# Kernel optimization log

Measured on AMD Instinct MI355X. Metric: run time of the kernel, lower is better.

Reference implementation:

```python
import jax, jax.numpy as jnp
import numpy as np

# ---- static hash-grid config (mirrors init_kwargs) ----
RANGE = 1.0
DIM = 3
N_LEVELS = 16
F_PER_LEVEL = 2
LOG2_HASHMAP = 15
HASHMAP_SIZE = 1 << LOG2_HASHMAP
BASE_RES = 16
FINEST_RES = 512
RANK = 4
PRIMES = np.array([1, 2654435761, 805459861], dtype=np.uint32)


def _resolutions():
    # N_l = floor(base * b^l), b = exp((ln(Nmax)-ln(Nmin))/(L-1))  (Instant-NGP eq. 2-3)
    b = np.exp((np.log(FINEST_RES) - np.log(BASE_RES)) / (N_LEVELS - 1))
    return np.floor(BASE_RES * b ** np.arange(N_LEVELS)).astype(np.float32)


def setup_inputs() -> dict:
    key = jax.random.key(0)
    k1, k2, k3 = jax.random.split(key, 3)
    x = jax.random.uniform(k1, (524288, DIM), dtype=jnp.float32)  # in [-range, range]
    # LoRA factors; small init like hash-grid tables (~1e-2 scale)
    table_A = jax.random.normal(k2, (N_LEVELS, HASHMAP_SIZE, RANK), dtype=jnp.float32) * 1e-2
    table_B = jax.random.normal(k3, (N_LEVELS, RANK, F_PER_LEVEL), dtype=jnp.float32) * 1e-1
    return {"x": x, "table_A": table_A, "table_B": table_B}


def reference(x, table_A, table_B):
    # wrapper: normalize to [0,1]
    xn = (x + RANGE) / (2.0 * RANGE)                         # [N,3]
    res = jnp.asarray(_resolutions())                        # [L]

    # materialize tiny per-level tables from LoRA factors: [L, S, F]
    tables = jnp.einsum('lsr,lrf->lsf', table_A, table_B)

    xl = xn[None, :, :] * res[:, None, None]                 # [L,N,3]
    xf = jnp.floor(xl)
    w = xl - xf                                              # [L,N,3] trilinear weights
    xi = xf.astype(jnp.uint32)                               # [L,N,3]

    # 2^3 corner offsets
    corners = jnp.array([[(c >> d) & 1 for d in range(DIM)] for c in range(2 ** DIM)],
                        dtype=jnp.uint32)                    # [8,3]

    pos = xi[:, :, None, :] + corners[None, None, :, :]      # [L,N,8,3]
    primes = jnp.asarray(PRIMES)
    h = (pos[..., 0] * primes[0]) ^ (pos[..., 1] * primes[1]) ^ (pos[..., 2] * primes[2])
    idx = (h & jnp.uint32(HASHMAP_SIZE - 1)).astype(jnp.int32)  # [L,N,8]

    # per-level gather: [L,N,8,F]
    feats = jax.vmap(lambda t, i: t[i])(tables, idx)

    # trilinear weights per corner: prod over dims of (w or 1-w)
    wc = jnp.prod(jnp.where(corners[None, None, :, :] == 1,
                            w[:, :, None, :], 1.0 - w[:, :, None, :]), axis=-1)  # [L,N,8]

    out_l = jnp.sum(feats * wc[..., None], axis=2)           # [L,N,F]
    out = jnp.transpose(out_l, (1, 0, 2)).reshape(x.shape[0], N_LEVELS * F_PER_LEVEL)
    return out.astype(jnp.float32)
```

## Files before the change

kernel.cpp:

```cpp
#include <hip/hip_runtime.h>
#include <hip/hip_fp16.h>
#include <math.h>
#include <stdint.h>
#include <stddef.h>

#define NLEVELS 16
#define HSIZE   32768
#define LOGH    15
#define RANKK   4
#define PRIME1  2654435761u
#define PRIME2  805459861u

#define BLK   1024
#define PPB   16384
#define UN    4
#define ITERS (PPB / (UN * BLK))

struct ResArr { float v[NLEVELS]; };

__device__ __forceinline__ void fma_mix_lo(float& acc, uint32_t pk, float w) {
    asm("v_fma_mix_f32 %0, %1, %2, %0 op_sel:[0,0,0] op_sel_hi:[1,0,0]"
        : "+v"(acc) : "v"(pk), "v"(w));
}
__device__ __forceinline__ void fma_mix_hi(float& acc, uint32_t pk, float w) {
    asm("v_fma_mix_f32 %0, %1, %2, %0 op_sel:[1,0,0] op_sel_hi:[1,0,0]"
        : "+v"(acc) : "v"(pk), "v"(w));
}

__global__ void build_tables_k(const float* __restrict__ A, const float* __restrict__ B,
                               uint32_t* __restrict__ T) {
    int i = blockIdx.x * blockDim.x + threadIdx.x;
    if (i >= NLEVELS * HSIZE) return;
    int l = i >> LOGH;
    const float4 a = *reinterpret_cast<const float4*>(A + (size_t)i * RANKK);
    const float* b = B + l * (RANKK * 2);
    float f0 = a.x * b[0] + a.y * b[2] + a.z * b[4] + a.w * b[6];
    float f1 = a.x * b[1] + a.y * b[3] + a.z * b[5] + a.w * b[7];
    __half2 h = __floats2half2_rn(f0, f1);
    T[i] = *reinterpret_cast<uint32_t*>(&h);
}

__global__ __launch_bounds__(BLK) __attribute__((amdgpu_waves_per_eu(4, 4)))
void encode_pair_k(const float* __restrict__ x, const uint32_t* __restrict__ T,
                   float* __restrict__ out, int nPoints, int nChunks, ResArr res) {
    __shared__ uint32_t lds[HSIZE];
    const int chunk = blockIdx.x % nChunks;
    const int pair  = blockIdx.x / nChunks;
    const int t     = threadIdx.x;
    const int base  = chunk * PPB;

    float2 r0[UN * ITERS];

#pragma unroll 1
    for (int phase = 0; phase < 2; ++phase) {
        const int l = 2 * pair + phase;
        {
            const uint4* Tl4 = reinterpret_cast<const uint4*>(T + (size_t)l * HSIZE);
            uint4* lds4 = reinterpret_cast<uint4*>(lds);
#pragma unroll
            for (int k = 0; k < HSIZE / 4 / BLK; ++k)
                lds4[k * BLK + t] = Tl4[k * BLK + t];
        }
        __syncthreads();

        const float r = res.v[l];

#pragma unroll
        for (int it = 0; it < ITERS; ++it) {
            int   n[UN];
            bool  ok[UN];
            float acc0[UN], acc1[UN];
            float w2v[UN], w2a_[UN];
            float wxy00[UN], wxy10[UN], wxy01[UN], wxy11[UN];
            uint32_t hx0[UN], hx1[UN], hy0[UN], hy1[UN], hz0[UN], hz1[UN];

#pragma unroll
            for (int u = 0; u < UN; ++u) {
                n[u]  = base + it * (UN * BLK) + u * BLK + t;
                ok[u] = (n[u] < nPoints);
                int m = ok[u] ? n[u] : 0;
                float xn0 = (x[3 * m + 0] + 1.0f) * 0.5f;
                float xn1 = (x[3 * m + 1] + 1.0f) * 0.5f;
                float xn2 = (x[3 * m + 2] + 1.0f) * 0.5f;
                float xl0 = xn0 * r, xl1 = xn1 * r, xl2 = xn2 * r;
                float fl0 = floorf(xl0), fl1 = floorf(xl1), fl2 = floorf(xl2);
                float w0 = xl0 - fl0, w1 = xl1 - fl1, w2 = xl2 - fl2;
                uint32_t i0 = (uint32_t)fl0, i1 = (uint32_t)fl1, i2 = (uint32_t)fl2;

                hx0[u] = i0;          hx1[u] = i0 + 1u;
                hy0[u] = i1 * PRIME1; hy1[u] = hy0[u] + PRIME1;
                hz0[u] = i2 * PRIME2; hz1[u] = hz0[u] + PRIME2;

                float w0a = 1.0f - w0, w1a = 1.0f - w1;
                w2v[u] = w2; w2a_[u] = 1.0f - w2;
                wxy00[u] = w0a * w1a; wxy10[u] = w0 * w1a;
                wxy01[u] = w0a * w1;  wxy11[u] = w0 * w1;
                acc0[u] = 0.0f; acc1[u] = 0.0f;
            }

#pragma unroll
            for (int c = 0; c < 8; ++c) {
#pragma unroll
                for (int u = 0; u < UN; ++u) {
                    uint32_t h = ((c & 1) ? hx1[u] : hx0[u]) ^ ((c & 2) ? hy1[u] : hy0[u])
                               ^ ((c & 4) ? hz1[u] : hz0[u]);
                    uint32_t pk = lds[h & (HSIZE - 1)];
                    float wxy = (c & 2) ? ((c & 1) ? wxy11[u] : wxy01[u])
                                        : ((c & 1) ? wxy10[u] : wxy00[u]);
                    float wc = wxy * ((c & 4) ? w2v[u] : w2a_[u]);
                    fma_mix_lo(acc0[u], pk, wc);
                    fma_mix_hi(acc1[u], pk, wc);
                }
            }

#pragma unroll
            for (int u = 0; u < UN; ++u) {
                if (phase == 0) {
                    r0[UN * it + u] = make_float2(acc0[u], acc1[u]);
                } else if (ok[u]) {
                    float2 p0 = r0[UN * it + u];
                    float4 v = make_float4(p0.x, p0.y, acc0[u], acc1[u]);
                    *reinterpret_cast<float4*>(out + (size_t)n[u] * 32 + 4 * pair) = v;
                }
            }
        }
        __syncthreads();
    }
}

__global__ void encode_fallback_k(const float* __restrict__ x, const float* __restrict__ A,
                                  const float* __restrict__ B, float* __restrict__ out,
                                  int nPoints, ResArr res) {
    int n = blockIdx.x * blockDim.x + threadIdx.x;
    if (n >= nPoints) return;
    float xn0 = (x[3 * n + 0] + 1.0f) * 0.5f;
    float xn1 = (x[3 * n + 1] + 1.0f) * 0.5f;
    float xn2 = (x[3 * n + 2] + 1.0f) * 0.5f;
    for (int l = 0; l < NLEVELS; ++l) {
        float r = res.v[l];
        float xl0 = xn0 * r, xl1 = xn1 * r, xl2 = xn2 * r;
        float fl0 = floorf(xl0), fl1 = floorf(xl1), fl2 = floorf(xl2);
        float w0 = xl0 - fl0, w1 = xl1 - fl1, w2 = xl2 - fl2;
        uint32_t i0 = (uint32_t)fl0, i1 = (uint32_t)fl1, i2 = (uint32_t)fl2;
        uint32_t hx0 = i0,          hx1 = i0 + 1u;
        uint32_t hy0 = i1 * PRIME1, hy1 = hy0 + PRIME1;
        uint32_t hz0 = i2 * PRIME2, hz1 = hz0 + PRIME2;
        float w0a = 1.0f - w0, w1a = 1.0f - w1, w2a = 1.0f - w2;
        float wxy00 = w0a * w1a, wxy10 = w0 * w1a, wxy01 = w0a * w1, wxy11 = w0 * w1;
        const float* b = B + l * 8;
        float b00 = b[0], b01 = b[1], b10 = b[2], b11 = b[3];
        float b20 = b[4], b21 = b[5], b30 = b[6], b31 = b[7];
        float acc0 = 0.0f, acc1 = 0.0f;
#pragma unroll
        for (int c = 0; c < 8; ++c) {
            uint32_t h = ((c & 1) ? hx1 : hx0) ^ ((c & 2) ? hy1 : hy0) ^ ((c & 4) ? hz1 : hz0);
            uint32_t idx = h & (HSIZE - 1);
            float4 a = *reinterpret_cast<const float4*>(A + ((size_t)l * HSIZE + idx) * RANKK);
            float fe0 = a.x * b00 + a.y * b10 + a.z * b20 + a.w * b30;
            float fe1 = a.x * b01 + a.y * b11 + a.z * b21 + a.w * b31;
            float wxy = (c & 2) ? ((c & 1) ? wxy11 : wxy01) : ((c & 1) ? wxy10 : wxy00);
            float wc = wxy * ((c & 4) ? w2 : w2a);
            acc0 = fmaf(fe0, wc, acc0);
            acc1 = fmaf(fe1, wc, acc1);
        }
        out[(size_t)n * 32 + 2 * l + 0] = acc0;
        out[(size_t)n * 32 + 2 * l + 1] = acc1;
    }
}

extern "C" void kernel_launch(void* const* d_in, const int* in_sizes, int n_in,
                              void* d_out, int out_size, void* d_ws, size_t ws_size,
                              hipStream_t stream) {
    const float* x = (const float*)d_in[0];
    const float* A = (const float*)d_in[1];
    const float* B = (const float*)d_in[2];
    float* out = (float*)d_out;
    int nPoints = in_sizes[0] / 3;

    ResArr ra;
    {
        double b = exp((log(512.0) - log(16.0)) / 15.0);
        for (int l = 0; l < NLEVELS; ++l)
            ra.v[l] = (float)floor(16.0 * pow(b, (double)l));
    }

    const size_t tblBytes = (size_t)NLEVELS * HSIZE * sizeof(uint32_t);

    if (ws_size >= tblBytes) {
        uint32_t* T = (uint32_t*)d_ws;
        int nb1 = (NLEVELS * HSIZE + 255) / 256;
        build_tables_k<<<nb1, 256, 0, stream>>>(A, B, T);
        int chunks = (nPoints + PPB - 1) / PPB;
        encode_pair_k<<<chunks * (NLEVELS / 2), BLK, 0, stream>>>(x, T, out, nPoints, chunks, ra);
    } else {
        encode_fallback_k<<<(nPoints + 255) / 256, 256, 0, stream>>>(x, A, B, out, nPoints, ra);
    }
}
```

Before: 136.7 us.

## Split pair-level blocks into single-level blocks with templated bounds checks

Each block now handles one level instead of two, which doubles the grid and removes the per-thread register buffer holding the first level's results along with the second table reload and barrier. A template flag drops bounds checks when the point count divides evenly into chunks, and the unroll factor falls from 4 to 2 with a runtime loop unrolled by 2. The cost is half-width float2 output stores instead of float4, so each 128-byte row is written in more, smaller pieces, plus an LDS table fill for every level block.

Result: faster. 128.9 us (-5.7%).

```diff
diff --git a/kernel.cpp b/kernel.cpp
--- a/kernel.cpp
+++ b/kernel.cpp
@@ -11,10 +11,9 @@
 #define PRIME1  2654435761u
 #define PRIME2  805459861u
 
-#define BLK   1024
-#define PPB   16384
-#define UN    4
-#define ITERS (PPB / (UN * BLK))
+#define BLK  1024
+#define PPB  16384
+#define UN   2
 
 struct ResArr { float v[NLEVELS]; };
 
@@ -40,91 +39,82 @@
     T[i] = *reinterpret_cast<uint32_t*>(&h);
 }
 
+template<bool FULL>
 __global__ __launch_bounds__(BLK) __attribute__((amdgpu_waves_per_eu(4, 4)))
-void encode_pair_k(const float* __restrict__ x, const uint32_t* __restrict__ T,
-                   float* __restrict__ out, int nPoints, int nChunks, ResArr res) {
+void encode_level_k(const float* __restrict__ x, const uint32_t* __restrict__ T,
+                    float* __restrict__ out, int nPoints, int nChunks, ResArr res) {
     __shared__ uint32_t lds[HSIZE];
     const int chunk = blockIdx.x % nChunks;
-    const int pair  = blockIdx.x / nChunks;
+    const int l     = blockIdx.x / nChunks;
     const int t     = threadIdx.x;
-    const int base  = chunk * PPB;
 
-    float2 r0[UN * ITERS];
+    {
+        const uint4* Tl4 = reinterpret_cast<const uint4*>(T + (size_t)l * HSIZE);
+        uint4* lds4 = reinterpret_cast<uint4*>(lds);
+#pragma unroll
+        for (int k = 0; k < HSIZE / 4 / BLK; ++k)
+            lds4[k * BLK + t] = Tl4[k * BLK + t];
+    }
+    __syncthreads();
 
-#pragma unroll 1
-    for (int phase = 0; phase < 2; ++phase) {
-        const int l = 2 * pair + phase;
-        {
-            const uint4* Tl4 = reinterpret_cast<const uint4*>(T + (size_t)l * HSIZE);
-            uint4* lds4 = reinterpret_cast<uint4*>(lds);
-#pragma unroll
-            for (int k = 0; k < HSIZE / 4 / BLK; ++k)
-                lds4[k * BLK + t] = Tl4[k * BLK + t];
-        }
-        __syncthreads();
+    const float r = res.v[l];
+    const int base = chunk * PPB;
 
-        const float r = res.v[l];
+#pragma unroll 2
+    for (int k = 0; k < PPB; k += UN * BLK) {
+        int   n[UN];
+        bool  ok[UN];
+        float acc0[UN], acc1[UN];
+        float w2v[UN], w2a_[UN];
+        float wxy00[UN], wxy10[UN], wxy01[UN], wxy11[UN];
+        uint32_t hx0[UN], hx1[UN], hy0[UN], hy1[UN], hz0[UN], hz1[UN];
 
 #pragma unroll
-        for (int it = 0; it < ITERS; ++it) {
-            int   n[UN];
-            bool  ok[UN];
-            float acc0[UN], acc1[UN];
-            float w2v[UN], w2a_[UN];
-            float wxy00[UN], wxy10[UN], wxy01[UN], wxy11[UN];
-            uint32_t hx0[UN], hx1[UN], hy0[UN], hy1[UN], hz0[UN], hz1[UN];
+        for (int u = 0; u < UN; ++u) {
+            n[u]  = base + k + u * BLK + t;
+            ok[u] = FULL || (n[u] < nPoints);
+            int m = FULL ? n[u] : (ok[u] ? n[u] : 0);
+            float xn0 = (x[3 * m + 0] + 1.0f) * 0.5f;
+            float xn1 = (x[3 * m + 1] + 1.0f) * 0.5f;
+            float xn2 = (x[3 * m + 2] + 1.0f) * 0.5f;
+            float xl0 = xn0 * r, xl1 = xn1 * r, xl2 = xn2 * r;
+            float fl0 = floorf(xl0), fl1 = floorf(xl1), fl2 = floorf(xl2);
+            float w0 = xl0 - fl0, w1 = xl1 - fl1, w2 = xl2 - fl2;
+            uint32_t i0 = (uint32_t)fl0, i1 = (uint32_t)fl1, i2 = (uint32_t)fl2;
+
+            hx0[u] = i0;          hx1[u] = i0 + 1u;
+            hy0[u] = i1 * PRIME1; hy1[u] = hy0[u] + PRIME1;
+            hz0[u] = i2 * PRIME2; hz1[u] = hz0[u] + PRIME2;
+
+            float w0a = 1.0f - w0, w1a = 1.0f - w1;
+            w2v[u] = w2; w2a_[u] = 1.0f - w2;
+            wxy00[u] = w0a * w1a; wxy10[u] = w0 * w1a;
+            wxy01[u] = w0a * w1;  wxy11[u] = w0 * w1;
+            acc0[u] = 0.0f; acc1[u] = 0.0f;
+        }
 
 #pragma unroll
+        for (int c = 0; c < 8; ++c) {
+#pragma unroll
             for (int u = 0; u < UN; ++u) {
-                n[u]  = base + it * (UN * BLK) + u * BLK + t;
-                ok[u] = (n[u] < nPoints);
-                int m = ok[u] ? n[u] : 0;
-                float xn0 = (x[3 * m + 0] + 1.0f) * 0.5f;
-                float xn1 = (x[3 * m + 1] + 1.0f) * 0.5f;
-                float xn2 = (x[3 * m + 2] + 1.0f) * 0.5f;
-                float xl0 = xn0 * r, xl1 = xn1 * r, xl2 = xn2 * r;
-                float fl0 = floorf(xl0), fl1 = floorf(xl1), fl2 = floorf(xl2);
-                float w0 = xl0 - fl0, w1 = xl1 - fl1, w2 = xl2 - fl2;
-                uint32_t i0 = (uint32_t)fl0, i1 = (uint32_t)fl1, i2 = (uint32_t)fl2;
-
-                hx0[u] = i0;          hx1[u] = i0 + 1u;
-                hy0[u] = i1 * PRIME1; hy1[u] = hy0[u] + PRIME1;
-                hz0[u] = i2 * PRIME2; hz1[u] = hz0[u] + PRIME2;
-
-                float w0a = 1.0f - w0, w1a = 1.0f - w1;
-                w2v[u] = w2; w2a_[u] = 1.0f - w2;
-                wxy00[u] = w0a * w1a; wxy10[u] = w0 * w1a;
-                wxy01[u] = w0a * w1;  wxy11[u] = w0 * w1;
-                acc0[u] = 0.0f; acc1[u] = 0.0f;
+                uint32_t h = ((c & 1) ? hx1[u] : hx0[u]) ^ ((c & 2) ? hy1[u] : hy0[u])
+                           ^ ((c & 4) ? hz1[u] : hz0[u]);
+                uint32_t pk = lds[h & (HSIZE - 1)];
+                float wxy = (c & 2) ? ((c & 1) ? wxy11[u] : wxy01[u])
+                                    : ((c & 1) ? wxy10[u] : wxy00[u]);
+                float wc = wxy * ((c & 4) ? w2v[u] : w2a_[u]);
+                fma_mix_lo(acc0[u], pk, wc);
+                fma_mix_hi(acc1[u], pk, wc);
             }
+        }
 
 #pragma unroll
-            for (int c = 0; c < 8; ++c) {
-#pragma unroll
-                for (int u = 0; u < UN; ++u) {
-                    uint32_t h = ((c & 1) ? hx1[u] : hx0[u]) ^ ((c & 2) ? hy1[u] : hy0[u])
-                               ^ ((c & 4) ? hz1[u] : hz0[u]);
-                    uint32_t pk = lds[h & (HSIZE - 1)];
-                    float wxy = (c & 2) ? ((c & 1) ? wxy11[u] : wxy01[u])
-                                        : ((c & 1) ? wxy10[u] : wxy00[u]);
-                    float wc = wxy * ((c & 4) ? w2v[u] : w2a_[u]);
-                    fma_mix_lo(acc0[u], pk, wc);
-                    fma_mix_hi(acc1[u], pk, wc);
-                }
-            }
-
-#pragma unroll
-            for (int u = 0; u < UN; ++u) {
-                if (phase == 0) {
-                    r0[UN * it + u] = make_float2(acc0[u], acc1[u]);
-                } else if (ok[u]) {
-                    float2 p0 = r0[UN * it + u];
-                    float4 v = make_float4(p0.x, p0.y, acc0[u], acc1[u]);
-                    *reinterpret_cast<float4*>(out + (size_t)n[u] * 32 + 4 * pair) = v;
-                }
+        for (int u = 0; u < UN; ++u) {
+            if (FULL || ok[u]) {
+                *reinterpret_cast<float2*>(out + (size_t)n[u] * 32 + 2 * l) =
+                    make_float2(acc0[u], acc1[u]);
             }
         }
-        __syncthreads();
     }
 }
 
@@ -191,7 +181,13 @@
         int nb1 = (NLEVELS * HSIZE + 255) / 256;
         build_tables_k<<<nb1, 256, 0, stream>>>(A, B, T);
         int chunks = (nPoints + PPB - 1) / PPB;
-        encode_pair_k<<<chunks * (NLEVELS / 2), BLK, 0, stream>>>(x, T, out, nPoints, chunks, ra);
+        if (nPoints % PPB == 0) {
+            encode_level_k<true><<<chunks * NLEVELS, BLK, 0, stream>>>(
+                x, T, out, nPoints, chunks, ra);
+        } else {
+            encode_level_k<false><<<chunks * NLEVELS, BLK, 0, stream>>>(
+                x, T, out, nPoints, chunks, ra);
+        }
     } else {
         encode_fallback_k<<<(nPoints + 255) / 256, 256, 0, stream>>>(x, A, B, out, nPoints, ra);
     }
```
